# Performance work log

Measured on AMD Instinct MI355X. Metric: run time of the kernel, lower is better.

## Reference

```python
import jax, jax.numpy as jnp
import numpy as np

D_MODEL = 1024


def setup_inputs() -> dict:
    key = jax.random.key(0)
    ks = jax.random.split(key, 7)
    d = D_MODEL
    x = jax.random.normal(ks[0], (4, 2048, d), dtype=jnp.float32)
    scale = 1.0 / np.sqrt(d)
    Wq = jax.random.normal(ks[1], (d, d), dtype=jnp.float32) * scale
    bq = jax.random.normal(ks[2], (d,), dtype=jnp.float32) * 0.01
    Wk = jax.random.normal(ks[3], (d, d), dtype=jnp.float32) * scale
    bk = jax.random.normal(ks[4], (d,), dtype=jnp.float32) * 0.01
    Wo = jax.random.normal(ks[5], (d, 1), dtype=jnp.float32) * scale
    bo = jax.random.normal(ks[6], (1,), dtype=jnp.float32) * 0.01
    return {"x": x, "Wq": Wq, "bq": bq, "Wk": Wk, "bk": bk, "Wo": Wo, "bo": bo}


def reference(x, Wq, bq, Wk, bk, Wo, bo):
    # x: [B, N, d]
    Q = x @ Wq + bq                      # [B, N, d]
    K = x @ Wk + bk                      # [B, N, d]
    scale = x.shape[-1] ** (-0.5)
    content_logits = jnp.einsum('bnd,bmd->bnm', Q, K) * scale  # [B, N, N]
    s = (x @ Wo + bo)[..., 0]            # [B, N]
    # ordering_bias[b, i, j] = tanh(s[b, j] - s[b, i]) * 5
    ordering_bias = jnp.tanh(s[:, None, :] - s[:, :, None]) * 5.0
    return content_logits + ordering_bias
```

## Files before the change

### kernel.cpp

```cpp
#include <hip/hip_runtime.h>
#include <math.h>

#define D_MODEL 1024
#define SEQ 2048
#define SCALE 0.03125f

using bf16x8 = __attribute__((ext_vector_type(8))) short;
using f32x4  = __attribute__((ext_vector_type(4))) float;

__device__ __forceinline__ unsigned short f2bf(float f) {
  union { float f; unsigned int u; } v; v.f = f;
  return (unsigned short)((v.u + 0x7fffu + ((v.u >> 16) & 1u)) >> 16);
}

__device__ __forceinline__ void async_cp16(const void* g, void* l) {
  __builtin_amdgcn_global_load_lds(
      (const __attribute__((address_space(1))) void*)g,
      (__attribute__((address_space(3))) void*)l, 16, 0, 0);
}

__device__ __forceinline__ const unsigned short* stage_ptr(
    const unsigned short* base, int row0, int ld, int tid) {
  const int r0 = tid >> 2;
  const int s0 = ((tid & 3) ^ ((r0 >> 1) & 3)) * 8;
  return base + (size_t)(row0 + r0) * ld + s0;
}

__device__ __forceinline__ void gemm_core(
    const unsigned short* __restrict__ gA, const unsigned short* __restrict__ gB,
    int lda, int ldb, unsigned short* As, unsigned short* Bs, int tid,
    f32x4 acc[4][4]) {
  const int lane = tid & 63, w = tid >> 6;
  const int wm = w >> 1, wn = w & 1;
  const int l16 = lane & 15, quad = lane >> 4;

  async_cp16(gA,            As + tid * 8);
  async_cp16(gA + 64 * lda, As + 2048 + tid * 8);
  async_cp16(gB,            Bs + tid * 8);
  async_cp16(gB + 64 * ldb, Bs + 2048 + tid * 8);
  __syncthreads();

  #pragma unroll 2
  for (int kk = 0; kk < 32; ++kk) {
    const int cur = (kk & 1) * 4096;
    const int nxt = 4096 - cur;
    if (kk < 31) {
      const unsigned short* a = gA + (kk + 1) * 32;
      const unsigned short* b = gB + (kk + 1) * 32;
      async_cp16(a,            As + nxt + tid * 8);
      async_cp16(a + 64 * lda, As + nxt + 2048 + tid * 8);
      async_cp16(b,            Bs + nxt + tid * 8);
      async_cp16(b + 64 * ldb, Bs + nxt + 2048 + tid * 8);
    }
    bf16x8 afr[4], bfr[4];
    #pragma unroll
    for (int mt = 0; mt < 4; mt++) {
      const int R = wm * 64 + mt * 16 + l16;
      afr[mt] = *(const bf16x8*)(As + cur + (R * 4 + (quad ^ ((R >> 1) & 3))) * 8);
    }
    #pragma unroll
    for (int nt = 0; nt < 4; nt++) {
      const int R = wn * 64 + nt * 16 + l16;
      bfr[nt] = *(const bf16x8*)(Bs + cur + (R * 4 + (quad ^ ((R >> 1) & 3))) * 8);
    }
    #pragma unroll
    for (int mt = 0; mt < 4; mt++)
      #pragma unroll
      for (int nt = 0; nt < 4; nt++)
        acc[mt][nt] = __builtin_amdgcn_mfma_f32_16x16x32_bf16(
            afr[mt], bfr[nt], acc[mt][nt], 0, 0, 0);
    __syncthreads();
  }
}

__device__ __forceinline__ void store_c_bf16(f32x4 acc[4][4],
                                             unsigned short* C, int ldc,
                                             int m0, int n0, int tid) {
  const int lane = tid & 63, w = tid >> 6;
  const int wm = w >> 1, wn = w & 1;
  const int l16 = lane & 15, quad = lane >> 4;
  #pragma unroll
  for (int mt = 0; mt < 4; mt++) {
    #pragma unroll
    for (int r = 0; r < 4; r++) {
      const int row = m0 + wm * 64 + mt * 16 + quad * 4 + r;
      unsigned short* cp = C + (size_t)row * ldc + n0 + wn * 64 + l16;
      #pragma unroll
      for (int nt = 0; nt < 4; nt++) cp[nt * 16] = f2bf(acc[mt][nt][r]);
    }
  }
}

__global__ __launch_bounds__(256) void wcvt_kernel(
    const float* __restrict__ Wq, const float* __restrict__ Wk,
    const float* __restrict__ bq, const float* __restrict__ bk,
    unsigned short* __restrict__ Wqb, unsigned short* __restrict__ Wkb,
    float* __restrict__ u, float* __restrict__ v, float* __restrict__ sc) {
  const int blk = blockIdx.x, tid = threadIdx.x;
  __shared__ float red[4];
  float p;
  if (blk < 2048) {
    const bool isq = blk < 1024;
    const int row = blk & 1023;
    const float* W = isq ? Wq : Wk;
    const float* bias = isq ? bk : bq;
    const float4 wv = ((const float4*)(W + (size_t)row * D_MODEL))[tid];
    const float4 bv = ((const float4*)bias)[tid];
    ushort4 o;
    o.x = f2bf(wv.x); o.y = f2bf(wv.y); o.z = f2bf(wv.z); o.w = f2bf(wv.w);
    ((ushort4*)((isq ? Wqb : Wkb) + (size_t)row * D_MODEL))[tid] = o;
    p = wv.x * bv.x + wv.y * bv.y + wv.z * bv.z + wv.w * bv.w;
    #pragma unroll
    for (int off = 32; off > 0; off >>= 1) p += __shfl_down(p, off, 64);
    if ((tid & 63) == 0) red[tid >> 6] = p;
    __syncthreads();
    if (tid == 0) (isq ? u : v)[row] = red[0] + red[1] + red[2] + red[3];
  } else {
    const float4 a = ((const float4*)bq)[tid];
    const float4 b = ((const float4*)bk)[tid];
    p = a.x * b.x + a.y * b.y + a.z * b.z + a.w * b.w;
    #pragma unroll
    for (int off = 32; off > 0; off >>= 1) p += __shfl_down(p, off, 64);
    if ((tid & 63) == 0) red[tid >> 6] = p;
    __syncthreads();
    if (tid == 0) sc[0] = SCALE * (red[0] + red[1] + red[2] + red[3]);
  }
}

__global__ __launch_bounds__(256) void prep_x_kernel(
    const float* __restrict__ x, const float* __restrict__ Wo,
    const float* __restrict__ bo, const float* __restrict__ u,
    const float* __restrict__ v, const float* __restrict__ sc,
    unsigned short* __restrict__ xb, float* __restrict__ tb,
    float* __restrict__ aa, float* __restrict__ bb) {
  const int m = blockIdx.x, tid = threadIdx.x;
  const float4 xv = ((const float4*)(x + (size_t)m * D_MODEL))[tid];
  const float4 wv = ((const float4*)Wo)[tid];
  const float4 uv = ((const float4*)u)[tid];
  const float4 vv = ((const float4*)v)[tid];
  ushort4 o;
  o.x = f2bf(xv.x); o.y = f2bf(xv.y); o.z = f2bf(xv.z); o.w = f2bf(xv.w);
  ((ushort4*)(xb + (size_t)m * D_MODEL))[tid] = o;
  float p0 = xv.x * wv.x + xv.y * wv.y + xv.z * wv.z + xv.w * wv.w;
  float p1 = xv.x * uv.x + xv.y * uv.y + xv.z * uv.z + xv.w * uv.w;
  float p2 = xv.x * vv.x + xv.y * vv.y + xv.z * vv.z + xv.w * vv.w;
  #pragma unroll
  for (int off = 32; off > 0; off >>= 1) {
    p0 += __shfl_down(p0, off, 64);
    p1 += __shfl_down(p1, off, 64);
    p2 += __shfl_down(p2, off, 64);
  }
  __shared__ float red[3][4];
  if ((tid & 63) == 0) {
    red[0][tid >> 6] = p0; red[1][tid >> 6] = p1; red[2][tid >> 6] = p2;
  }
  __syncthreads();
  if (tid == 0) {
    tb[m] = tanhf(red[0][0] + red[0][1] + red[0][2] + red[0][3] + bo[0]);
    aa[m] = SCALE * (red[1][0] + red[1][1] + red[1][2] + red[1][3]) + sc[0];
    bb[m] = SCALE * (red[2][0] + red[2][1] + red[2][2] + red[2][3]);
  }
}

__global__ __launch_bounds__(256, 3) void wmm_kernel(
    const unsigned short* __restrict__ Wkb,
    const unsigned short* __restrict__ Wqb, unsigned short* __restrict__ Mt) {
  const int m0 = blockIdx.x * 128, n0 = blockIdx.y * 128;
  __shared__ unsigned short As[2 * 4096], Bs[2 * 4096];
  const int tid = threadIdx.x;
  f32x4 acc[4][4];
  #pragma unroll
  for (int i = 0; i < 4; i++)
    #pragma unroll
    for (int j = 0; j < 4; j++) acc[i][j] = f32x4{0.f, 0.f, 0.f, 0.f};
  gemm_core(stage_ptr(Wkb, m0, D_MODEL, tid), stage_ptr(Wqb, n0, D_MODEL, tid),
            D_MODEL, D_MODEL, As, Bs, tid, acc);
  store_c_bf16(acc, Mt, D_MODEL, m0, n0, tid);
}

__global__ __launch_bounds__(256, 3) void zgen_kernel(
    const unsigned short* __restrict__ xb,
    const unsigned short* __restrict__ Mt, unsigned short* __restrict__ Zb) {
  const int m0 = blockIdx.x * 128, n0 = blockIdx.y * 128;
  __shared__ unsigned short As[2 * 4096], Bs[2 * 4096];
  const int tid = threadIdx.x;
  f32x4 acc[4][4];
  #pragma unroll
  for (int i = 0; i < 4; i++)
    #pragma unroll
    for (int j = 0; j < 4; j++) acc[i][j] = f32x4{0.f, 0.f, 0.f, 0.f};
  gemm_core(stage_ptr(xb, m0, D_MODEL, tid), stage_ptr(Mt, n0, D_MODEL, tid),
            D_MODEL, D_MODEL, As, Bs, tid, acc);
  store_c_bf16(acc, Zb, D_MODEL, m0, n0, tid);
}

__global__ __launch_bounds__(256, 3) void zxt_kernel(
    const unsigned short* __restrict__ Zb, const unsigned short* __restrict__ xb,
    const float* __restrict__ tb, const float* __restrict__ aa,
    const float* __restrict__ bb, float* __restrict__ out) {
  const int b = blockIdx.z;
  const int i0 = blockIdx.x * 128, j0 = blockIdx.y * 128;
  __shared__ unsigned short As[2 * 4096], Bs[2 * 4096];
  __shared__ float tsi[128], tsj[128], tsa[128], tsb[128];
  const int tid = threadIdx.x;
  if (tid < 128) {
    tsi[tid] = tb[b * SEQ + i0 + tid];
    tsa[tid] = aa[b * SEQ + i0 + tid];
  } else {
    tsj[tid - 128] = tb[b * SEQ + j0 + tid - 128];
    tsb[tid - 128] = bb[b * SEQ + j0 + tid - 128];
  }
  f32x4 acc[4][4];
  #pragma unroll
  for (int i = 0; i < 4; i++)
    #pragma unroll
    for (int j = 0; j < 4; j++) acc[i][j] = f32x4{0.f, 0.f, 0.f, 0.f};
  const unsigned short* A = Zb + (size_t)b * SEQ * D_MODEL;
  const unsigned short* Bt = xb + (size_t)b * SEQ * D_MODEL;
  gemm_core(stage_ptr(A, i0, D_MODEL, tid), stage_ptr(Bt, j0, D_MODEL, tid),
            D_MODEL, D_MODEL, As, Bs, tid, acc);

  const int lane = tid & 63, w = tid >> 6;
  const int wm = w >> 1, wn = w & 1;
  const int l16 = lane & 15, quad = lane >> 4;
  float tj[4], bj[4];
  #pragma unroll
  for (int nt = 0; nt < 4; nt++) {
    tj[nt] = tsj[wn * 64 + nt * 16 + l16];
    bj[nt] = tsb[wn * 64 + nt * 16 + l16];
  }
  #pragma unroll
  for (int mt = 0; mt < 4; mt++) {
    #pragma unroll
    for (int r = 0; r < 4; r++) {
      const int il = wm * 64 + mt * 16 + quad * 4 + r;
      const float ti = tsi[il];
      const float ai = tsa[il];
      float* cp = out + ((size_t)(b * SEQ + i0 + il)) * SEQ + j0 + wn * 64 + l16;
      #pragma unroll
      for (int nt = 0; nt < 4; nt++) {
        const float num = tj[nt] - ti;
        const float den = fmaf(-tj[nt], ti, 1.0f);
        const float obias = 5.0f * num * __builtin_amdgcn_rcpf(den);
        cp[nt * 16] = SCALE * acc[mt][nt][r] + ai + bj[nt] + obias;
      }
    }
  }
}

extern "C" void kernel_launch(void* const* d_in, const int* in_sizes, int n_in,
                              void* d_out, int out_size, void* d_ws, size_t ws_size,
                              hipStream_t stream) {
  const float* x  = (const float*)d_in[0];
  const float* Wq = (const float*)d_in[1];
  const float* bq = (const float*)d_in[2];
  const float* Wk = (const float*)d_in[3];
  const float* bk = (const float*)d_in[4];
  const float* Wo = (const float*)d_in[5];
  const float* bo = (const float*)d_in[6];
  float* out = (float*)d_out;

  char* ws = (char*)d_ws;
  unsigned short* xb  = (unsigned short*)(ws);
  unsigned short* Zb  = (unsigned short*)(ws + (16ull << 20));
  unsigned short* Wqb = (unsigned short*)(ws + (32ull << 20));
  unsigned short* Wkb = (unsigned short*)(ws + (34ull << 20));
  unsigned short* Mt  = (unsigned short*)(ws + (36ull << 20));
  float* tb = (float*)(ws + (38ull << 20));
  float* aa = (float*)(ws + (38ull << 20) + (32ull << 10));
  float* bb = (float*)(ws + (38ull << 20) + (64ull << 10));
  float* u  = (float*)(ws + (38ull << 20) + (96ull << 10));
  float* v  = (float*)(ws + (38ull << 20) + (100ull << 10));
  float* sc = (float*)(ws + (38ull << 20) + (104ull << 10));

  wcvt_kernel<<<2049, 256, 0, stream>>>(Wq, Wk, bq, bk, Wqb, Wkb, u, v, sc);
  prep_x_kernel<<<8192, 256, 0, stream>>>(x, Wo, bo, u, v, sc, xb, tb, aa, bb);
  wmm_kernel<<<dim3(8, 8), 256, 0, stream>>>(Wkb, Wqb, Mt);
  zgen_kernel<<<dim3(64, 8), 256, 0, stream>>>(xb, Mt, Zb);
  zxt_kernel<<<dim3(16, 16, 4), 256, 0, stream>>>(Zb, xb, tb, aa, bb, out);
}
```

Measured before the change: 195.2 us.

## Merge prep kernels and compute row projections as extra GEMM column tile

Merges the weight-conversion and x-conversion kernels into a single launch, so the x conversion no longer waits on the u/v vectors. The three per-row dot products (x·Wo, x·u, x·v) are no longer done as fp32 reductions in the prep kernel. Instead they are packed as three bf16 rows of a special B matrix and computed as a ninth column tile of the zgen GEMM. This removes one launch and the serial dependency, but it lowers the precision of the bias and score terms to bf16. It also spends a full 128-wide tile of MFMA work on only three useful columns, and that tile reads B rows beyond the three filled Wsp rows.

```diff
diff --git a/kernel.cpp b/kernel.cpp
--- a/kernel.cpp
+++ b/kernel.cpp
@@ -91,17 +91,25 @@
   }
 }
 
-__global__ __launch_bounds__(256) void wcvt_kernel(
-    const float* __restrict__ Wq, const float* __restrict__ Wk,
-    const float* __restrict__ bq, const float* __restrict__ bk,
-    unsigned short* __restrict__ Wqb, unsigned short* __restrict__ Wkb,
-    float* __restrict__ u, float* __restrict__ v, float* __restrict__ sc) {
-  const int blk = blockIdx.x, tid = threadIdx.x;
+__global__ __launch_bounds__(256) void prep_kernel(
+    const float* __restrict__ x, const float* __restrict__ Wq,
+    const float* __restrict__ Wk, const float* __restrict__ bq,
+    const float* __restrict__ bk, const float* __restrict__ Wo,
+    unsigned short* __restrict__ xb, unsigned short* __restrict__ Wqb,
+    unsigned short* __restrict__ Wkb, unsigned short* __restrict__ Wsp,
+    float* __restrict__ sc) {
+  const int bid = blockIdx.x, tid = threadIdx.x;
+  if (bid < 8192) {
+    const float4 xv = ((const float4*)(x + (size_t)bid * D_MODEL))[tid];
+    ushort4 o;
+    o.x = f2bf(xv.x); o.y = f2bf(xv.y); o.z = f2bf(xv.z); o.w = f2bf(xv.w);
+    ((ushort4*)(xb + (size_t)bid * D_MODEL))[tid] = o;
+    return;
+  }
   __shared__ float red[4];
-  float p;
-  if (blk < 2048) {
-    const bool isq = blk < 1024;
-    const int row = blk & 1023;
+  if (bid < 10240) {
+    const bool isq = bid < 9216;
+    const int row = bid - (isq ? 8192 : 9216);
     const float* W = isq ? Wq : Wk;
     const float* bias = isq ? bk : bq;
     const float4 wv = ((const float4*)(W + (size_t)row * D_MODEL))[tid];
@@ -109,57 +117,27 @@
     ushort4 o;
     o.x = f2bf(wv.x); o.y = f2bf(wv.y); o.z = f2bf(wv.z); o.w = f2bf(wv.w);
     ((ushort4*)((isq ? Wqb : Wkb) + (size_t)row * D_MODEL))[tid] = o;
-    p = wv.x * bv.x + wv.y * bv.y + wv.z * bv.z + wv.w * bv.w;
+    float p = wv.x * bv.x + wv.y * bv.y + wv.z * bv.z + wv.w * bv.w;
     #pragma unroll
     for (int off = 32; off > 0; off >>= 1) p += __shfl_down(p, off, 64);
     if ((tid & 63) == 0) red[tid >> 6] = p;
     __syncthreads();
-    if (tid == 0) (isq ? u : v)[row] = red[0] + red[1] + red[2] + red[3];
-  } else {
-    const float4 a = ((const float4*)bq)[tid];
-    const float4 b = ((const float4*)bk)[tid];
-    p = a.x * b.x + a.y * b.y + a.z * b.z + a.w * b.w;
-    #pragma unroll
-    for (int off = 32; off > 0; off >>= 1) p += __shfl_down(p, off, 64);
-    if ((tid & 63) == 0) red[tid >> 6] = p;
-    __syncthreads();
-    if (tid == 0) sc[0] = SCALE * (red[0] + red[1] + red[2] + red[3]);
-  }
-}
-
-__global__ __launch_bounds__(256) void prep_x_kernel(
-    const float* __restrict__ x, const float* __restrict__ Wo,
-    const float* __restrict__ bo, const float* __restrict__ u,
-    const float* __restrict__ v, const float* __restrict__ sc,
-    unsigned short* __restrict__ xb, float* __restrict__ tb,
-    float* __restrict__ aa, float* __restrict__ bb) {
-  const int m = blockIdx.x, tid = threadIdx.x;
-  const float4 xv = ((const float4*)(x + (size_t)m * D_MODEL))[tid];
-  const float4 wv = ((const float4*)Wo)[tid];
-  const float4 uv = ((const float4*)u)[tid];
-  const float4 vv = ((const float4*)v)[tid];
+    if (tid == 0)
+      Wsp[(isq ? 0 : D_MODEL) + row] = f2bf(red[0] + red[1] + red[2] + red[3]);
+    return;
+  }
+  const float4 a = ((const float4*)bq)[tid];
+  const float4 b = ((const float4*)bk)[tid];
+  float p = a.x * b.x + a.y * b.y + a.z * b.z + a.w * b.w;
+  #pragma unroll
+  for (int off = 32; off > 0; off >>= 1) p += __shfl_down(p, off, 64);
+  if ((tid & 63) == 0) red[tid >> 6] = p;
+  __syncthreads();
+  if (tid == 0) sc[0] = SCALE * (red[0] + red[1] + red[2] + red[3]);
+  const float4 wo = ((const float4*)Wo)[tid];
   ushort4 o;
-  o.x = f2bf(xv.x); o.y = f2bf(xv.y); o.z = f2bf(xv.z); o.w = f2bf(xv.w);
-  ((ushort4*)(xb + (size_t)m * D_MODEL))[tid] = o;
-  float p0 = xv.x * wv.x + xv.y * wv.y + xv.z * wv.z + xv.w * wv.w;
-  float p1 = xv.x * uv.x + xv.y * uv.y + xv.z * uv.z + xv.w * uv.w;
-  float p2 = xv.x * vv.x + xv.y * vv.y + xv.z * vv.z + xv.w * vv.w;
-  #pragma unroll
-  for (int off = 32; off > 0; off >>= 1) {
-    p0 += __shfl_down(p0, off, 64);
-    p1 += __shfl_down(p1, off, 64);
-    p2 += __shfl_down(p2, off, 64);
-  }
-  __shared__ float red[3][4];
-  if ((tid & 63) == 0) {
-    red[0][tid >> 6] = p0; red[1][tid >> 6] = p1; red[2][tid >> 6] = p2;
-  }
-  __syncthreads();
-  if (tid == 0) {
-    tb[m] = tanhf(red[0][0] + red[0][1] + red[0][2] + red[0][3] + bo[0]);
-    aa[m] = SCALE * (red[1][0] + red[1][1] + red[1][2] + red[1][3]) + sc[0];
-    bb[m] = SCALE * (red[2][0] + red[2][1] + red[2][2] + red[2][3]);
-  }
+  o.x = f2bf(wo.x); o.y = f2bf(wo.y); o.z = f2bf(wo.z); o.w = f2bf(wo.w);
+  ((ushort4*)(Wsp + 2 * D_MODEL))[tid] = o;
 }
 
 __global__ __launch_bounds__(256, 3) void wmm_kernel(
@@ -180,8 +158,14 @@
 
 __global__ __launch_bounds__(256, 3) void zgen_kernel(
     const unsigned short* __restrict__ xb,
-    const unsigned short* __restrict__ Mt, unsigned short* __restrict__ Zb) {
-  const int m0 = blockIdx.x * 128, n0 = blockIdx.y * 128;
+    const unsigned short* __restrict__ Mt,
+    const unsigned short* __restrict__ Wsp, const float* __restrict__ scp,
+    const float* __restrict__ bo, unsigned short* __restrict__ Zb,
+    float* __restrict__ aa, float* __restrict__ bb, float* __restrict__ tb) {
+  const int m0 = blockIdx.x * 128;
+  const bool special = (blockIdx.y == 8);
+  const unsigned short* Bbase = special ? Wsp : Mt;
+  const int n0 = special ? 0 : blockIdx.y * 128;
   __shared__ unsigned short As[2 * 4096], Bs[2 * 4096];
   const int tid = threadIdx.x;
   f32x4 acc[4][4];
@@ -189,9 +173,28 @@
   for (int i = 0; i < 4; i++)
     #pragma unroll
     for (int j = 0; j < 4; j++) acc[i][j] = f32x4{0.f, 0.f, 0.f, 0.f};
-  gemm_core(stage_ptr(xb, m0, D_MODEL, tid), stage_ptr(Mt, n0, D_MODEL, tid),
+  gemm_core(stage_ptr(xb, m0, D_MODEL, tid), stage_ptr(Bbase, n0, D_MODEL, tid),
             D_MODEL, D_MODEL, As, Bs, tid, acc);
-  store_c_bf16(acc, Zb, D_MODEL, m0, n0, tid);
+  if (!special) {
+    store_c_bf16(acc, Zb, D_MODEL, m0, n0, tid);
+    return;
+  }
+  const int lane = tid & 63, w = tid >> 6;
+  const int wm = w >> 1, wn = w & 1;
+  const int l16 = lane & 15, quad = lane >> 4;
+  if (wn) return;
+  const float scv = scp[0], bov = bo[0];
+  #pragma unroll
+  for (int mt = 0; mt < 4; mt++) {
+    #pragma unroll
+    for (int r = 0; r < 4; r++) {
+      const int row = m0 + wm * 64 + mt * 16 + quad * 4 + r;
+      const float val = acc[mt][0][r];
+      if (l16 == 0)      aa[row] = SCALE * val + scv;
+      else if (l16 == 1) bb[row] = SCALE * val;
+      else if (l16 == 2) tb[row] = tanhf(val + bov);
+    }
+  }
 }
 
 __global__ __launch_bounds__(256, 3) void zxt_kernel(
@@ -266,16 +269,16 @@
   unsigned short* Wqb = (unsigned short*)(ws + (32ull << 20));
   unsigned short* Wkb = (unsigned short*)(ws + (34ull << 20));
   unsigned short* Mt  = (unsigned short*)(ws + (36ull << 20));
-  float* tb = (float*)(ws + (38ull << 20));
-  float* aa = (float*)(ws + (38ull << 20) + (32ull << 10));
-  float* bb = (float*)(ws + (38ull << 20) + (64ull << 10));
-  float* u  = (float*)(ws + (38ull << 20) + (96ull << 10));
-  float* v  = (float*)(ws + (38ull << 20) + (100ull << 10));
-  float* sc = (float*)(ws + (38ull << 20) + (104ull << 10));
-
-  wcvt_kernel<<<2049, 256, 0, stream>>>(Wq, Wk, bq, bk, Wqb, Wkb, u, v, sc);
-  prep_x_kernel<<<8192, 256, 0, stream>>>(x, Wo, bo, u, v, sc, xb, tb, aa, bb);
+  unsigned short* Wsp = (unsigned short*)(ws + (38ull << 20));
+  float* tb = (float*)(ws + (38ull << 20) + (256ull << 10));
+  float* aa = (float*)(ws + (38ull << 20) + (288ull << 10));
+  float* bb = (float*)(ws + (38ull << 20) + (320ull << 10));
+  float* sc = (float*)(ws + (38ull << 20) + (352ull << 10));
+
+  prep_kernel<<<10241, 256, 0, stream>>>(x, Wq, Wk, bq, bk, Wo,
+                                         xb, Wqb, Wkb, Wsp, sc);
   wmm_kernel<<<dim3(8, 8), 256, 0, stream>>>(Wkb, Wqb, Mt);
-  zgen_kernel<<<dim3(64, 8), 256, 0, stream>>>(xb, Mt, Zb);
+  zgen_kernel<<<dim3(64, 9), 256, 0, stream>>>(xb, Mt, Wsp, sc, bo,
+                                               Zb, aa, bb, tb);
   zxt_kernel<<<dim3(16, 16, 4), 256, 0, stream>>>(Zb, xb, tb, aa, bb, out);
 }
```

Measured after the change: 197.0 us. Within noise of the previous version (+0.9%).
